# Kernel tuning notes

Hardware: AMD Instinct MI355X
Metric: run time of the kernel (lower is better)

The kernel has to match this reference:

```python
import jax, jax.numpy as jnp
import numpy as np
import math

NX = 240
XL = 6.0
A_ORB = 2
V0 = -20.0
S_INT = 0.5
ITERMAX = 500
FFAC = 0.4


def _wfho(n, x):
    # harmonic-oscillator eigenfunction (numpy, setup only)
    nfac = math.factorial(n)
    norm = (2.0 ** n * nfac) ** (-0.5) / math.pi ** 0.25
    if n == 0:
        Hn = np.ones_like(x)
    elif n == 1:
        Hn = 2.0 * x
    else:
        hm2 = np.ones_like(x)
        hm1 = 2.0 * x
        for m in range(2, n + 1):
            hmx = 2.0 * x * hm1 - 2.0 * (m - 1) * hm2
            hm2, hm1 = hm1, hmx
        Hn = hmx
    return norm * np.exp(-x ** 2 / 2.0) * Hn


def setup_inputs() -> dict:
    delx = 2.0 * XL / NX
    xx = delx * (np.arange(NX) - NX / 2.0)
    delp = 2.0 * math.pi / (2.0 * XL)
    pp = delp * (np.arange(NX) - NX / 2.0)
    # cder2[i,j] = sum_k exp(1j*(xj-xi)*pp_k) * pp_k^2 ; only real part is used
    D = xx[None, :] - xx[:, None]                      # [Nx, Nx], xj - xi
    cder2_re = np.cos(D[:, :, None] * pp[None, None, :]) @ (pp ** 2)
    der2 = -cder2_re * delx * delp / (2.0 * math.pi)
    kin = -der2 / 2.0
    pfac = 1.0 / abs(kin.max())
    U_HO = xx ** 2 / 2.0
    x1, x2 = np.meshgrid(xx, xx, indexing='ij')
    Vint = V0 * (2.0 * math.pi) ** (-0.5) / S_INT * np.exp(-(x1 - x2) ** 2 / (2.0 * S_INT ** 2))
    wfy0 = np.stack([_wfho(n, xx) for n in range(A_ORB)], axis=1)  # [Nx, Nmax]
    return {
        'wfy0': jnp.asarray(wfy0, jnp.float32),
        'kin_mat': jnp.asarray(kin, jnp.float32),
        'Vint': jnp.asarray(Vint, jnp.float32),
        'U_HO': jnp.asarray(U_HO, jnp.float32),
        'delx': jnp.float32(delx),
        'pfac': jnp.float32(pfac),
        'itermax': ITERMAX,
    }


def reference(wfy0, kin_mat, Vint, U_HO, delx, pfac, itermax):
    Nmax = wfy0.shape[1]
    delx = jnp.asarray(delx, jnp.float32).reshape(())
    pfac = jnp.asarray(pfac, jnp.float32).reshape(())

    def step(wfy, _):
        # densities from current orbitals
        hf_den = jnp.sum(wfy ** 2, axis=1)            # [Nx]
        hf_den_mat = wfy @ wfy.T                      # [Nx, Nx]
        Udir = delx * (Vint @ hf_den)
        Umf_mat = -delx * Vint * hf_den_mat
        Umf_mat = Umf_mat + jnp.diag(Udir + U_HO)     # add to diagonal
        H = kin_mat + Umf_mat

        updated = []
        spe = []
        ekin = jnp.float32(0.0)
        epot = jnp.float32(0.0)
        for ieig in range(Nmax):                      # Nmax=2, unrolled
            wf0 = wfy[:, ieig]
            wff = H @ wf0
            spe.append((wf0 @ wff) * delx)
            wfb = wf0 - wff * pfac
            norm = jnp.sum(wfb ** 2) * delx
            wff = wfb / jnp.sqrt(norm)
            for jeig in range(ieig):                  # Gram-Schmidt vs already-updated orbitals
                wff = wff - updated[jeig] * (updated[jeig] @ wff) * delx
            norm = jnp.sum(wff ** 2) * delx
            wff = wff / norm                          # faithful: divide by norm (not sqrt)
            new = FFAC * wff + (1.0 - FFAC) * wf0
            updated.append(new)
            ekin = ekin + (new @ (kin_mat @ new)) * delx
            epot = epot + (new @ (Umf_mat @ new)) * delx
        wfy_new = jnp.stack(updated, axis=1)

        esum0hf = spe[0]
        for s_ in spe[1:]:
            esum0hf = esum0hf + s_
        eho = jnp.sum(hf_den * U_HO) * delx / 2.0
        enerhfp = (esum0hf + ekin) / 2.0 + eho
        epot0hf = epot - 2.0 * eho
        enerhf = esum0hf - epot0hf / 2.0
        out = jnp.stack([enerhf, enerhfp, ekin, eho, epot0hf, esum0hf])
        return wfy_new, out

    _, outs = jax.lax.scan(step, wfy0, None, length=int(itermax))
    return outs[-1]  # (enerhf, enerhfp, ekin0hf, eho, epot0hf, esum0hf)
```

## Files before the change

kernel.cpp:

```cpp
#include <hip/hip_runtime.h>


#define NXX  240
#define NPAD 256
#define NTH  512
#define KJCH 60
#define KNB  15

typedef _Float16 h2 __attribute__((ext_vector_type(2)));

__device__ __forceinline__ h2 bch2(unsigned u) { union { unsigned u; h2 h; } c; c.u = u; return c.h; }
__device__ __forceinline__ unsigned bcu(h2 h)  { union { unsigned u; h2 h; } c; c.h = h; return c.u; }
__device__ __forceinline__ unsigned pkh(float a, float b) {
  h2 p; p.x = (_Float16)a; p.y = (_Float16)b; return bcu(p);
}

__device__ __forceinline__ float fdot2(h2 a, h2 b, float c) {
#if __has_builtin(__builtin_amdgcn_fdot2)
  return __builtin_amdgcn_fdot2(a, b, c, false);
#else
  float d;
  asm("v_dot2_f32_f16 %0, %1, %2, %3" : "=v"(d) : "v"(a), "v"(b), "v"(c));
  return d;
#endif
}

__device__ __forceinline__ float wdw(const float4* w, int idx) {
  const float4 q = w[idx >> 2];
  const int c = idx & 3;
  return c == 0 ? q.x : (c == 1 ? q.y : (c == 2 ? q.z : q.w));
}

template <int CTRL, int N>
__device__ __forceinline__ void dppStepN(float (&v)[N]) {
#pragma unroll
  for (int k = 0; k < N; ++k) {
    int s = __builtin_amdgcn_update_dpp(0, __float_as_int(v[k]), CTRL, 0xF, 0xF, false);
    v[k] += __int_as_float(s);
  }
}
template <int N>
__device__ __forceinline__ void waveSumDppN(float (&v)[N]) {
  dppStepN<0xB1>(v);
  dppStepN<0x4E>(v);
  dppStepN<0x141>(v);
  dppStepN<0x140>(v);
  dppStepN<0x142>(v);
  dppStepN<0x143>(v);
#pragma unroll
  for (int k = 0; k < N; ++k)
    v[k] = __int_as_float(__builtin_amdgcn_readlane(__float_as_int(v[k]), 63));
}

struct __align__(16) Smem {
  float cK[512];
  unsigned pkV[512];
  float uho[NPAD];
  float wfb[2][2][NPAD];
  unsigned xpk[3][NPAD/2];
  unsigned xprk[4][NPAD/2];
  float part[4][6][NPAD];
};

__device__ __forceinline__ void kinConv(const float* x0p, const float* x1p, int jg,
                                        const float4* cw, float (&a0)[4], float (&a1)[4]) {
#pragma unroll
  for (int b = 0; b < KNB; ++b) {
    const int j0 = jg + 4 * b;
    const float4 x0 = *(const float4*)&x0p[j0];
    const float4 x1 = *(const float4*)&x1p[j0];
    const float4 kh = cw[15 - b], kl = cw[14 - b];
    const float ck[8] = {kl.x, kl.y, kl.z, kl.w, kh.x, kh.y, kh.z, kh.w};
    const float xs0[4] = {x0.x, x0.y, x0.z, x0.w};
    const float xs1[4] = {x1.x, x1.y, x1.z, x1.w};
#pragma unroll
    for (int s = 0; s < 4; ++s)
#pragma unroll
      for (int r = 0; r < 4; ++r) {
        const int c = 4 + r - s;
        a0[r] = fmaf(xs0[s], ck[c], a0[r]);
        a1[r] = fmaf(xs1[s], ck[c], a1[r]);
      }
  }
}

template <int NSB>
__device__ __forceinline__ void vConv3(const unsigned* q0, const unsigned* q1,
                                       const unsigned* q2, int jgp,
                                       const float4* win, float (&A)[3][4]) {
#pragma unroll
  for (int sb = 0; sb < NSB; ++sb) {
    const int base = jgp + 4 * sb;
    const uint4 X0 = *(const uint4*)&q0[base];
    const uint4 X1 = *(const uint4*)&q1[base];
    const uint4 X2 = *(const uint4*)&q2[base];
    const unsigned xs0[4] = {X0.x, X0.y, X0.z, X0.w};
    const unsigned xs1[4] = {X1.x, X1.y, X1.z, X1.w};
    const unsigned xs2[4] = {X2.x, X2.y, X2.z, X2.w};
#pragma unroll
    for (int p = 0; p < 4; ++p)
#pragma unroll
      for (int r = 0; r < 4; ++r) {
        const int di = r - 2 * p - 8 * sb + (NSB * 8 - 2) + 2;
        const h2 c = bch2(__float_as_uint(wdw(win, di)));
        A[0][r] = fdot2(c, bch2(xs0[p]), A[0][r]);
        A[1][r] = fdot2(c, bch2(xs1[p]), A[1][r]);
        A[2][r] = fdot2(c, bch2(xs2[p]), A[2][r]);
      }
  }
}

template <int NSB>
__device__ __forceinline__ void vConv4(const unsigned (*q)[NPAD / 2], int jgp,
                                       const float4* win, float (&A)[4][4]) {
#pragma unroll
  for (int sb = 0; sb < NSB; ++sb) {
    const int base = jgp + 4 * sb;
    const uint4 X0 = *(const uint4*)&q[0][base];
    const uint4 X1 = *(const uint4*)&q[1][base];
    const uint4 X2 = *(const uint4*)&q[2][base];
    const uint4 X3 = *(const uint4*)&q[3][base];
    const unsigned xs0[4] = {X0.x, X0.y, X0.z, X0.w};
    const unsigned xs1[4] = {X1.x, X1.y, X1.z, X1.w};
    const unsigned xs2[4] = {X2.x, X2.y, X2.z, X2.w};
    const unsigned xs3[4] = {X3.x, X3.y, X3.z, X3.w};
#pragma unroll
    for (int p = 0; p < 4; ++p)
#pragma unroll
      for (int r = 0; r < 4; ++r) {
        const int di = r - 2 * p - 8 * sb + (NSB * 8 - 2) + 2;
        const h2 c = bch2(__float_as_uint(wdw(win, di)));
        A[0][r] = fdot2(c, bch2(xs0[p]), A[0][r]);
        A[1][r] = fdot2(c, bch2(xs1[p]), A[1][r]);
        A[2][r] = fdot2(c, bch2(xs2[p]), A[2][r]);
        A[3][r] = fdot2(c, bch2(xs3[p]), A[3][r]);
      }
  }
}

__global__ void __launch_bounds__(NTH, 2)
hf_kernel(const float* __restrict__ wfy0,
          const float* __restrict__ kin,
          const float* __restrict__ vnt,
          const float* __restrict__ uho_g,
          const float* __restrict__ delx_p,
          const float* __restrict__ pfac_p,
          const int*   __restrict__ iter_p,
          float* __restrict__ out)
{
  __shared__ Smem sm;
  const int t  = (int)threadIdx.x;
  const int wv = t >> 6;
  const int l  = t & 63;
  const int i0 = 4 * l;
  const bool isK = (wv < 4);
  const int g  = isK ? wv : wv - 4;
  const int jgK = KJCH * g;
  const int jgV = 64 * g;
  const int lenV = (g < 3) ? 64 : 48;
  const float delx = delx_p[0];
  const float pfac = pfac_p[0];
  const int itermax = iter_p[0];

  for (int a = t; a < 512; a += NTH) {
    int d = a - 256;
    float vk = 0.f;
    if (d >= 0 && d < NXX)      vk = kin[(size_t)d * NXX];
    else if (d < 0 && -d < NXX) vk = kin[-d];
    sm.cK[a] = vk;
    float vh = 0.f, vl = 0.f;
    if (d >= 0 && d < NXX)      vh = vnt[(size_t)d * NXX];
    else if (d < 0 && -d < NXX) vh = vnt[-d];
    int d2 = d - 1;
    if (d2 >= 0 && d2 < NXX)      vl = vnt[(size_t)d2 * NXX];
    else if (d2 < 0 && -d2 < NXX) vl = vnt[-d2];
    sm.pkV[a] = pkh(vh, vl);
  }
  if (t < NPAD) {
    float u  = (t < NXX) ? uho_g[t]        : 0.f;
    float a0 = (t < NXX) ? wfy0[2 * t]     : 0.f;
    float a1 = (t < NXX) ? wfy0[2 * t + 1] : 0.f;
    sm.uho[t] = u;
    sm.wfb[0][0][t] = a0; sm.wfb[0][1][t] = a1;
    sm.wfb[1][0][t] = 0.f; sm.wfb[1][1][t] = 0.f;
  }
  if (t < NPAD / 2) {
    int j0 = 2 * t, j1 = 2 * t + 1;
    float w00 = (j0 < NXX) ? wfy0[2 * j0]     : 0.f;
    float w01 = (j0 < NXX) ? wfy0[2 * j0 + 1] : 0.f;
    float w10 = (j1 < NXX) ? wfy0[2 * j1]     : 0.f;
    float w11 = (j1 < NXX) ? wfy0[2 * j1 + 1] : 0.f;
    sm.xpk[0][t] = pkh(w00 * w00, w10 * w10);
    sm.xpk[1][t] = pkh(w00 * w01, w10 * w11);
    sm.xpk[2][t] = pkh(w01 * w01, w11 * w11);
  }
  __syncthreads();

  float4 winq[17];
  if (isK) {
    const int qb = l - 15 * g + 49;
#pragma unroll
    for (int m = 0; m < 16; ++m) winq[m] = *(const float4*)&sm.cK[4 * (qb + m)];
    winq[16] = make_float4(0.f, 0.f, 0.f, 0.f);
  } else {
    const int ab = i0 - jgV - lenV + 256;
#pragma unroll
    for (int m = 0; m < 17; ++m) {
      const uint4 q = *(const uint4*)&sm.pkV[ab + 4 * m];
      winq[m] = make_float4(__uint_as_float(q.x), __uint_as_float(q.y),
                            __uint_as_float(q.z), __uint_as_float(q.w));
    }
  }

  int cur = 0;
  for (int it = 0; it < itermax; ++it) {
    const bool last = (it == itermax - 1);
    const float* wf0 = sm.wfb[cur][0];
    const float* wf1 = sm.wfb[cur][1];
    float* nw0 = sm.wfb[cur ^ 1][0];
    float* nw1 = sm.wfb[cur ^ 1][1];

    if (isK) {
      float aK0[4] = {0, 0, 0, 0}, aK1[4] = {0, 0, 0, 0};
      kinConv(wf0, wf1, jgK, winq, aK0, aK1);
      *(float4*)&sm.part[g][0][i0] = make_float4(aK0[0], aK0[1], aK0[2], aK0[3]);
      *(float4*)&sm.part[g][1][i0] = make_float4(aK1[0], aK1[1], aK1[2], aK1[3]);
    } else {
      float aV[3][4] = {};
      if (g < 3) vConv3<8>(sm.xpk[0], sm.xpk[1], sm.xpk[2], jgV / 2, winq, aV);
      else       vConv3<6>(sm.xpk[0], sm.xpk[1], sm.xpk[2], jgV / 2, winq, aV);
#pragma unroll
      for (int c = 0; c < 3; ++c)
        *(float4*)&sm.part[g][2 + c][i0] =
            make_float4(aV[c][0], aV[c][1], aV[c][2], aV[c][3]);
    }
    __syncthreads();

    float w0[4], w1[4], Ut[4], wff0[4], wff1[4], new0[4], new1[4];
    float spe0 = 0.f, spe1 = 0.f, eho = 0.f;

    if (wv == 0) {
      const bool valid = (l < 60);
      float k0[4]  = {0, 0, 0, 0}, k1[4]  = {0, 0, 0, 0};
      float v00[4] = {0, 0, 0, 0}, v01[4] = {0, 0, 0, 0}, v11[4] = {0, 0, 0, 0};
#pragma unroll
      for (int gg = 0; gg < 4; ++gg) {
        const float4 A0 = *(const float4*)&sm.part[gg][0][i0];
        const float4 A1 = *(const float4*)&sm.part[gg][1][i0];
        const float4 A2 = *(const float4*)&sm.part[gg][2][i0];
        const float4 A3 = *(const float4*)&sm.part[gg][3][i0];
        const float4 A4 = *(const float4*)&sm.part[gg][4][i0];
        k0[0]  += A0.x; k0[1]  += A0.y; k0[2]  += A0.z; k0[3]  += A0.w;
        k1[0]  += A1.x; k1[1]  += A1.y; k1[2]  += A1.z; k1[3]  += A1.w;
        v00[0] += A2.x; v00[1] += A2.y; v00[2] += A2.z; v00[3] += A2.w;
        v01[0] += A3.x; v01[1] += A3.y; v01[2] += A3.z; v01[3] += A3.w;
        v11[0] += A4.x; v11[1] += A4.y; v11[2] += A4.z; v11[3] += A4.w;
      }
      const float4 w0q = *(const float4*)&wf0[i0];
      const float4 w1q = *(const float4*)&wf1[i0];
      const float4 uq  = *(const float4*)&sm.uho[i0];
      w0[0] = w0q.x; w0[1] = w0q.y; w0[2] = w0q.z; w0[3] = w0q.w;
      w1[0] = w1q.x; w1[1] = w1q.y; w1[2] = w1q.z; w1[3] = w1q.w;
      const float uh[4] = {uq.x, uq.y, uq.z, uq.w};

      float wb0[4], wb1[4];
      float red[6] = {0, 0, 0, 0, 0, 0};
#pragma unroll
      for (int r = 0; r < 4; ++r) {
        Ut[r]   = delx * (v00[r] + v11[r]) + uh[r];
        wff0[r] = k0[r] - delx * (w0[r] * v00[r] + w1[r] * v01[r]) + Ut[r] * w0[r];
        wff1[r] = k1[r] - delx * (w0[r] * v01[r] + w1[r] * v11[r]) + Ut[r] * w1[r];
        wb0[r]  = w0[r] - pfac * wff0[r];
        wb1[r]  = w1[r] - pfac * wff1[r];
        if (!valid) { wb0[r] = 0.f; wb1[r] = 0.f; }
        red[0] += wb0[r] * wb0[r];
        red[1] += wb1[r] * wb1[r];
        red[2] += wb0[r] * wb1[r];
        red[3] += w0[r]  * wb1[r];
        red[4] += wb0[r] * w0[r];
        red[5] += w0[r]  * w0[r];
      }
      waveSumDppN<6>(red);
      const float rdelx = 1.f / delx;
      const float inv0 = 1.f / sqrtf(red[0] * delx);
      const float inv1 = 1.f / sqrtf(red[1] * delx);
      const float dB = delx * inv1 * (0.4f * red[2] * inv0 + 0.6f * red[3]);
      const float e0 = 0.16f * rdelx + 0.48f * red[4] * inv0 + 0.36f * red[5];
      const float sB = rdelx - dB * dB * (2.f * rdelx - e0);
      const float invB = 1.f / (sB * delx);
#pragma unroll
      for (int r = 0; r < 4; ++r) {
        const float wfA  = wb0[r] * inv0;
        const float wfBp = wb1[r] * inv1;
        new0[r] = 0.4f * wfA + 0.6f * w0[r];
        const float wfB2 = wfBp - new0[r] * dB;
        new1[r] = 0.4f * wfB2 * invB + 0.6f * w1[r];
      }
      *(float4*)&nw0[i0] = make_float4(new0[0], new0[1], new0[2], new0[3]);
      *(float4*)&nw1[i0] = make_float4(new1[0], new1[1], new1[2], new1[3]);
      *(uint2*)&sm.xpk[0][2 * l] = make_uint2(
          pkh(new0[0] * new0[0], new0[1] * new0[1]),
          pkh(new0[2] * new0[2], new0[3] * new0[3]));
      *(uint2*)&sm.xpk[1][2 * l] = make_uint2(
          pkh(new0[0] * new1[0], new0[1] * new1[1]),
          pkh(new0[2] * new1[2], new0[3] * new1[3]));
      *(uint2*)&sm.xpk[2][2 * l] = make_uint2(
          pkh(new1[0] * new1[0], new1[1] * new1[1]),
          pkh(new1[2] * new1[2], new1[3] * new1[3]));

      if (last) {
        float er[3] = {0, 0, 0};
#pragma unroll
        for (int r = 0; r < 4; ++r) {
          er[0] += w0[r] * wff0[r];
          er[1] += w1[r] * wff1[r];
          er[2] += (w0[r] * w0[r] + w1[r] * w1[r]) * uh[r];
        }
        waveSumDppN<3>(er);
        spe0 = er[0] * delx; spe1 = er[1] * delx; eho = er[2] * delx * 0.5f;
      }
    }
    __syncthreads();

    if (last) {
      if (t < NPAD / 2) {
        const float2 o0 = *(const float2*)&wf0[2 * t];
        const float2 o1 = *(const float2*)&wf1[2 * t];
        const float2 n0 = *(const float2*)&nw0[2 * t];
        const float2 n1 = *(const float2*)&nw1[2 * t];
        sm.xprk[0][t] = pkh(o0.x * n0.x, o0.y * n0.y);
        sm.xprk[1][t] = pkh(o1.x * n0.x, o1.y * n0.y);
        sm.xprk[2][t] = pkh(o0.x * n1.x, o0.y * n1.y);
        sm.xprk[3][t] = pkh(o1.x * n1.x, o1.y * n1.y);
      }
      __syncthreads();

      if (isK) {
        float bA0[4] = {0, 0, 0, 0}, bA1[4] = {0, 0, 0, 0};
        kinConv(nw0, nw1, jgK, winq, bA0, bA1);
        *(float4*)&sm.part[g][0][i0] = make_float4(bA0[0], bA0[1], bA0[2], bA0[3]);
        *(float4*)&sm.part[g][1][i0] = make_float4(bA1[0], bA1[1], bA1[2], bA1[3]);
      } else {
        float bV[4][4] = {};
        if (g < 3) vConv4<8>(sm.xprk, jgV / 2, winq, bV);
        else       vConv4<6>(sm.xprk, jgV / 2, winq, bV);
#pragma unroll
        for (int c2 = 0; c2 < 4; ++c2)
          *(float4*)&sm.part[g][2 + c2][i0] =
              make_float4(bV[c2][0], bV[c2][1], bV[c2][2], bV[c2][3]);
      }
      __syncthreads();

      if (wv == 0) {
        float rd[6][4] = {};
#pragma unroll
        for (int gg = 0; gg < 4; ++gg)
#pragma unroll
          for (int c = 0; c < 6; ++c) {
            const float4 A = *(const float4*)&sm.part[gg][c][i0];
            rd[c][0] += A.x; rd[c][1] += A.y; rd[c][2] += A.z; rd[c][3] += A.w;
          }
        float er[2] = {0, 0};
#pragma unroll
        for (int r = 0; r < 4; ++r) {
          const float um0 = -delx * (w0[r] * rd[2][r] + w1[r] * rd[3][r]) + Ut[r] * new0[r];
          const float um1 = -delx * (w0[r] * rd[4][r] + w1[r] * rd[5][r]) + Ut[r] * new1[r];
          er[0] += new0[r] * rd[0][r] + new1[r] * rd[1][r];
          er[1] += new0[r] * um0 + new1[r] * um1;
        }
        waveSumDppN<2>(er);
        const float ekin = er[0] * delx, epot = er[1] * delx;
        if (l == 0) {
          const float esum    = spe0 + spe1;
          const float enerhfp = 0.5f * (esum + ekin) + eho;
          const float epot0hf = epot - 2.f * eho;
          const float enerhf  = esum - 0.5f * epot0hf;
          out[0] = enerhf; out[1] = enerhfp; out[2] = ekin;
          out[3] = eho;    out[4] = epot0hf; out[5] = esum;
        }
      }
    }
    cur ^= 1;
  }
}

extern "C" void kernel_launch(void* const* d_in, const int* in_sizes, int n_in,
                              void* d_out, int out_size, void* d_ws, size_t ws_size,
                              hipStream_t stream) {
  const float* wfy0 = (const float*)d_in[0];
  const float* kin  = (const float*)d_in[1];
  const float* vnt  = (const float*)d_in[2];
  const float* uho  = (const float*)d_in[3];
  const float* delx = (const float*)d_in[4];
  const float* pfac = (const float*)d_in[5];
  const int*   itm  = (const int*)d_in[6];
  hipLaunchKernelGGL(hf_kernel, dim3(1), dim3(NTH), 0, stream,
                     wfy0, kin, vnt, uho, delx, pfac, itm, (float*)d_out);
}
```

Baseline: 1.079 ms.

## Spread per-iteration orbital update across four waves with cross-wave reductions

Previously a single wave did the whole serial update phase each iteration: summing partials, the Hamiltonian application, Gram-Schmidt and normalization, with four grid points per lane. Now the four kinetic waves each own one point per lane. Their wave-level DPP reductions are combined through a small shared buffer, and the packed fp16 density arrays become per-element halfword stores. This shortens the serial critical path of the update phase and folds the last-iteration product packing into it. The cost is an extra __syncthreads and shared-memory round trips for the cross-wave reductions every iteration.

```diff
diff --git a/kernel.cpp b/kernel.cpp
--- a/kernel.cpp
+++ b/kernel.cpp
@@ -13,6 +13,9 @@
 __device__ __forceinline__ unsigned bcu(h2 h)  { union { unsigned u; h2 h; } c; c.h = h; return c.u; }
 __device__ __forceinline__ unsigned pkh(float a, float b) {
   h2 p; p.x = (_Float16)a; p.y = (_Float16)b; return bcu(p);
+}
+__device__ __forceinline__ unsigned short h16(float a) {
+  union { _Float16 h; unsigned short u; } c; c.h = (_Float16)a; return c.u;
 }
 
 __device__ __forceinline__ float fdot2(h2 a, h2 b, float c) {
@@ -57,9 +60,10 @@
   unsigned pkV[512];
   float uho[NPAD];
   float wfb[2][2][NPAD];
-  unsigned xpk[3][NPAD/2];
-  unsigned xprk[4][NPAD/2];
+  unsigned short xpkh[3][NPAD];
+  unsigned short xprkh[4][NPAD];
   float part[4][6][NPAD];
+  float redb[4][12];
 };
 
 __device__ __forceinline__ void kinConv(const float* x0p, const float* x1p, int jg,
@@ -158,6 +162,7 @@
   const int jgK = KJCH * g;
   const int jgV = 64 * g;
   const int lenV = (g < 3) ? 64 : 48;
+  const int r  = 64 * (wv & 3) + l;
   const float delx = delx_p[0];
   const float pfac = pfac_p[0];
   const int itermax = iter_p[0];
@@ -190,9 +195,9 @@
     float w01 = (j0 < NXX) ? wfy0[2 * j0 + 1] : 0.f;
     float w10 = (j1 < NXX) ? wfy0[2 * j1]     : 0.f;
     float w11 = (j1 < NXX) ? wfy0[2 * j1 + 1] : 0.f;
-    sm.xpk[0][t] = pkh(w00 * w00, w10 * w10);
-    sm.xpk[1][t] = pkh(w00 * w01, w10 * w11);
-    sm.xpk[2][t] = pkh(w01 * w01, w11 * w11);
+    ((unsigned*)sm.xpkh[0])[t] = pkh(w00 * w00, w10 * w10);
+    ((unsigned*)sm.xpkh[1])[t] = pkh(w00 * w01, w10 * w11);
+    ((unsigned*)sm.xpkh[2])[t] = pkh(w01 * w01, w11 * w11);
   }
   __syncthreads();
 
@@ -227,8 +232,10 @@
       *(float4*)&sm.part[g][1][i0] = make_float4(aK1[0], aK1[1], aK1[2], aK1[3]);
     } else {
       float aV[3][4] = {};
-      if (g < 3) vConv3<8>(sm.xpk[0], sm.xpk[1], sm.xpk[2], jgV / 2, winq, aV);
-      else       vConv3<6>(sm.xpk[0], sm.xpk[1], sm.xpk[2], jgV / 2, winq, aV);
+      if (g < 3) vConv3<8>((const unsigned*)sm.xpkh[0], (const unsigned*)sm.xpkh[1],
+                           (const unsigned*)sm.xpkh[2], jgV / 2, winq, aV);
+      else       vConv3<6>((const unsigned*)sm.xpkh[0], (const unsigned*)sm.xpkh[1],
+                           (const unsigned*)sm.xpkh[2], jgV / 2, winq, aV);
 #pragma unroll
       for (int c = 0; c < 3; ++c)
         *(float4*)&sm.part[g][2 + c][i0] =
@@ -236,105 +243,82 @@
     }
     __syncthreads();
 
-    float w0[4], w1[4], Ut[4], wff0[4], wff1[4], new0[4], new1[4];
+    float w0s = 0.f, w1s = 0.f, Uts = 0.f, wff0s = 0.f, wff1s = 0.f;
+    float wb0s = 0.f, wb1s = 0.f, new0s = 0.f, new1s = 0.f;
     float spe0 = 0.f, spe1 = 0.f, eho = 0.f;
 
-    if (wv == 0) {
-      const bool valid = (l < 60);
-      float k0[4]  = {0, 0, 0, 0}, k1[4]  = {0, 0, 0, 0};
-      float v00[4] = {0, 0, 0, 0}, v01[4] = {0, 0, 0, 0}, v11[4] = {0, 0, 0, 0};
+    if (isK) {
+      const bool valid = (r < NXX);
+      float k0 = 0.f, k1 = 0.f, v00 = 0.f, v01 = 0.f, v11 = 0.f;
 #pragma unroll
       for (int gg = 0; gg < 4; ++gg) {
-        const float4 A0 = *(const float4*)&sm.part[gg][0][i0];
-        const float4 A1 = *(const float4*)&sm.part[gg][1][i0];
-        const float4 A2 = *(const float4*)&sm.part[gg][2][i0];
-        const float4 A3 = *(const float4*)&sm.part[gg][3][i0];
-        const float4 A4 = *(const float4*)&sm.part[gg][4][i0];
-        k0[0]  += A0.x; k0[1]  += A0.y; k0[2]  += A0.z; k0[3]  += A0.w;
-        k1[0]  += A1.x; k1[1]  += A1.y; k1[2]  += A1.z; k1[3]  += A1.w;
-        v00[0] += A2.x; v00[1] += A2.y; v00[2] += A2.z; v00[3] += A2.w;
-        v01[0] += A3.x; v01[1] += A3.y; v01[2] += A3.z; v01[3] += A3.w;
-        v11[0] += A4.x; v11[1] += A4.y; v11[2] += A4.z; v11[3] += A4.w;
-      }
-      const float4 w0q = *(const float4*)&wf0[i0];
-      const float4 w1q = *(const float4*)&wf1[i0];
-      const float4 uq  = *(const float4*)&sm.uho[i0];
-      w0[0] = w0q.x; w0[1] = w0q.y; w0[2] = w0q.z; w0[3] = w0q.w;
-      w1[0] = w1q.x; w1[1] = w1q.y; w1[2] = w1q.z; w1[3] = w1q.w;
-      const float uh[4] = {uq.x, uq.y, uq.z, uq.w};
-
-      float wb0[4], wb1[4];
-      float red[6] = {0, 0, 0, 0, 0, 0};
-#pragma unroll
-      for (int r = 0; r < 4; ++r) {
-        Ut[r]   = delx * (v00[r] + v11[r]) + uh[r];
-        wff0[r] = k0[r] - delx * (w0[r] * v00[r] + w1[r] * v01[r]) + Ut[r] * w0[r];
-        wff1[r] = k1[r] - delx * (w0[r] * v01[r] + w1[r] * v11[r]) + Ut[r] * w1[r];
-        wb0[r]  = w0[r] - pfac * wff0[r];
-        wb1[r]  = w1[r] - pfac * wff1[r];
-        if (!valid) { wb0[r] = 0.f; wb1[r] = 0.f; }
-        red[0] += wb0[r] * wb0[r];
-        red[1] += wb1[r] * wb1[r];
-        red[2] += wb0[r] * wb1[r];
-        red[3] += w0[r]  * wb1[r];
-        red[4] += wb0[r] * w0[r];
-        red[5] += w0[r]  * w0[r];
-      }
+        k0  += sm.part[gg][0][r];
+        k1  += sm.part[gg][1][r];
+        v00 += sm.part[gg][2][r];
+        v01 += sm.part[gg][3][r];
+        v11 += sm.part[gg][4][r];
+      }
+      w0s = wf0[r]; w1s = wf1[r];
+      const float uhs = sm.uho[r];
+      Uts   = delx * (v00 + v11) + uhs;
+      wff0s = k0 - delx * (w0s * v00 + w1s * v01) + Uts * w0s;
+      wff1s = k1 - delx * (w0s * v01 + w1s * v11) + Uts * w1s;
+      wb0s  = w0s - pfac * wff0s;
+      wb1s  = w1s - pfac * wff1s;
+      if (!valid) { wb0s = 0.f; wb1s = 0.f; }
+      float red[6] = { wb0s * wb0s, wb1s * wb1s, wb0s * wb1s,
+                       w0s * wb1s,  wb0s * w0s,  w0s * w0s };
       waveSumDppN<6>(red);
+      if (l == 0) {
+#pragma unroll
+        for (int k = 0; k < 6; ++k) sm.redb[wv][k] = red[k];
+      }
+      if (last) {
+        float er[3] = { w0s * wff0s, w1s * wff1s,
+                        (w0s * w0s + w1s * w1s) * uhs };
+        waveSumDppN<3>(er);
+        if (l == 0) {
+          sm.redb[wv][6] = er[0]; sm.redb[wv][7] = er[1]; sm.redb[wv][8] = er[2];
+        }
+      }
+    }
+    __syncthreads();
+
+    if (isK) {
+      float rs[6];
+#pragma unroll
+      for (int k = 0; k < 6; ++k)
+        rs[k] = sm.redb[0][k] + sm.redb[1][k] + sm.redb[2][k] + sm.redb[3][k];
       const float rdelx = 1.f / delx;
-      const float inv0 = 1.f / sqrtf(red[0] * delx);
-      const float inv1 = 1.f / sqrtf(red[1] * delx);
-      const float dB = delx * inv1 * (0.4f * red[2] * inv0 + 0.6f * red[3]);
-      const float e0 = 0.16f * rdelx + 0.48f * red[4] * inv0 + 0.36f * red[5];
+      const float inv0 = 1.f / sqrtf(rs[0] * delx);
+      const float inv1 = 1.f / sqrtf(rs[1] * delx);
+      const float dB = delx * inv1 * (0.4f * rs[2] * inv0 + 0.6f * rs[3]);
+      const float e0 = 0.16f * rdelx + 0.48f * rs[4] * inv0 + 0.36f * rs[5];
       const float sB = rdelx - dB * dB * (2.f * rdelx - e0);
       const float invB = 1.f / (sB * delx);
-#pragma unroll
-      for (int r = 0; r < 4; ++r) {
-        const float wfA  = wb0[r] * inv0;
-        const float wfBp = wb1[r] * inv1;
-        new0[r] = 0.4f * wfA + 0.6f * w0[r];
-        const float wfB2 = wfBp - new0[r] * dB;
-        new1[r] = 0.4f * wfB2 * invB + 0.6f * w1[r];
-      }
-      *(float4*)&nw0[i0] = make_float4(new0[0], new0[1], new0[2], new0[3]);
-      *(float4*)&nw1[i0] = make_float4(new1[0], new1[1], new1[2], new1[3]);
-      *(uint2*)&sm.xpk[0][2 * l] = make_uint2(
-          pkh(new0[0] * new0[0], new0[1] * new0[1]),
-          pkh(new0[2] * new0[2], new0[3] * new0[3]));
-      *(uint2*)&sm.xpk[1][2 * l] = make_uint2(
-          pkh(new0[0] * new1[0], new0[1] * new1[1]),
-          pkh(new0[2] * new1[2], new0[3] * new1[3]));
-      *(uint2*)&sm.xpk[2][2 * l] = make_uint2(
-          pkh(new1[0] * new1[0], new1[1] * new1[1]),
-          pkh(new1[2] * new1[2], new1[3] * new1[3]));
-
+      const float wfA  = wb0s * inv0;
+      const float wfBp = wb1s * inv1;
+      new0s = 0.4f * wfA + 0.6f * w0s;
+      const float wfB2 = wfBp - new0s * dB;
+      new1s = 0.4f * wfB2 * invB + 0.6f * w1s;
+      nw0[r] = new0s;
+      nw1[r] = new1s;
+      sm.xpkh[0][r] = h16(new0s * new0s);
+      sm.xpkh[1][r] = h16(new0s * new1s);
+      sm.xpkh[2][r] = h16(new1s * new1s);
       if (last) {
-        float er[3] = {0, 0, 0};
-#pragma unroll
-        for (int r = 0; r < 4; ++r) {
-          er[0] += w0[r] * wff0[r];
-          er[1] += w1[r] * wff1[r];
-          er[2] += (w0[r] * w0[r] + w1[r] * w1[r]) * uh[r];
-        }
-        waveSumDppN<3>(er);
-        spe0 = er[0] * delx; spe1 = er[1] * delx; eho = er[2] * delx * 0.5f;
+        spe0 = (sm.redb[0][6] + sm.redb[1][6] + sm.redb[2][6] + sm.redb[3][6]) * delx;
+        spe1 = (sm.redb[0][7] + sm.redb[1][7] + sm.redb[2][7] + sm.redb[3][7]) * delx;
+        eho  = (sm.redb[0][8] + sm.redb[1][8] + sm.redb[2][8] + sm.redb[3][8]) * delx * 0.5f;
+        sm.xprkh[0][r] = h16(w0s * new0s);
+        sm.xprkh[1][r] = h16(w1s * new0s);
+        sm.xprkh[2][r] = h16(w0s * new1s);
+        sm.xprkh[3][r] = h16(w1s * new1s);
       }
     }
     __syncthreads();
 
     if (last) {
-      if (t < NPAD / 2) {
-        const float2 o0 = *(const float2*)&wf0[2 * t];
-        const float2 o1 = *(const float2*)&wf1[2 * t];
-        const float2 n0 = *(const float2*)&nw0[2 * t];
-        const float2 n1 = *(const float2*)&nw1[2 * t];
-        sm.xprk[0][t] = pkh(o0.x * n0.x, o0.y * n0.y);
-        sm.xprk[1][t] = pkh(o1.x * n0.x, o1.y * n0.y);
-        sm.xprk[2][t] = pkh(o0.x * n1.x, o0.y * n1.y);
-        sm.xprk[3][t] = pkh(o1.x * n1.x, o1.y * n1.y);
-      }
-      __syncthreads();
-
       if (isK) {
         float bA0[4] = {0, 0, 0, 0}, bA1[4] = {0, 0, 0, 0};
         kinConv(nw0, nw1, jgK, winq, bA0, bA1);
@@ -342,8 +326,10 @@
         *(float4*)&sm.part[g][1][i0] = make_float4(bA1[0], bA1[1], bA1[2], bA1[3]);
       } else {
         float bV[4][4] = {};
-        if (g < 3) vConv4<8>(sm.xprk, jgV / 2, winq, bV);
-        else       vConv4<6>(sm.xprk, jgV / 2, winq, bV);
+        const unsigned (*xq)[NPAD / 2] =
+            reinterpret_cast<const unsigned (*)[NPAD / 2]>(&sm.xprkh[0][0]);
+        if (g < 3) vConv4<8>(xq, jgV / 2, winq, bV);
+        else       vConv4<6>(xq, jgV / 2, winq, bV);
 #pragma unroll
         for (int c2 = 0; c2 < 4; ++c2)
           *(float4*)&sm.part[g][2 + c2][i0] =
@@ -351,33 +337,37 @@
       }
       __syncthreads();
 
-      if (wv == 0) {
-        float rd[6][4] = {};
-#pragma unroll
-        for (int gg = 0; gg < 4; ++gg)
-#pragma unroll
-          for (int c = 0; c < 6; ++c) {
-            const float4 A = *(const float4*)&sm.part[gg][c][i0];
-            rd[c][0] += A.x; rd[c][1] += A.y; rd[c][2] += A.z; rd[c][3] += A.w;
-          }
-        float er[2] = {0, 0};
-#pragma unroll
-        for (int r = 0; r < 4; ++r) {
-          const float um0 = -delx * (w0[r] * rd[2][r] + w1[r] * rd[3][r]) + Ut[r] * new0[r];
-          const float um1 = -delx * (w0[r] * rd[4][r] + w1[r] * rd[5][r]) + Ut[r] * new1[r];
-          er[0] += new0[r] * rd[0][r] + new1[r] * rd[1][r];
-          er[1] += new0[r] * um0 + new1[r] * um1;
+      if (isK) {
+        float kn0 = 0.f, kn1 = 0.f, u00 = 0.f, u01 = 0.f, u10 = 0.f, u11 = 0.f;
+#pragma unroll
+        for (int gg = 0; gg < 4; ++gg) {
+          kn0 += sm.part[gg][0][r];
+          kn1 += sm.part[gg][1][r];
+          u00 += sm.part[gg][2][r];
+          u01 += sm.part[gg][3][r];
+          u10 += sm.part[gg][4][r];
+          u11 += sm.part[gg][5][r];
         }
-        waveSumDppN<2>(er);
-        const float ekin = er[0] * delx, epot = er[1] * delx;
-        if (l == 0) {
-          const float esum    = spe0 + spe1;
-          const float enerhfp = 0.5f * (esum + ekin) + eho;
-          const float epot0hf = epot - 2.f * eho;
-          const float enerhf  = esum - 0.5f * epot0hf;
-          out[0] = enerhf; out[1] = enerhfp; out[2] = ekin;
-          out[3] = eho;    out[4] = epot0hf; out[5] = esum;
-        }
+        const float um0 = -delx * (w0s * u00 + w1s * u01) + Uts * new0s;
+        const float um1 = -delx * (w0s * u10 + w1s * u11) + Uts * new1s;
+        float er2[2] = { new0s * kn0 + new1s * kn1,
+                         new0s * um0 + new1s * um1 };
+        waveSumDppN<2>(er2);
+        if (l == 0) { sm.redb[wv][9] = er2[0]; sm.redb[wv][10] = er2[1]; }
+      }
+      __syncthreads();
+
+      if (t == 0) {
+        const float ekin = (sm.redb[0][9]  + sm.redb[1][9] +
+                            sm.redb[2][9]  + sm.redb[3][9])  * delx;
+        const float epot = (sm.redb[0][10] + sm.redb[1][10] +
+                            sm.redb[2][10] + sm.redb[3][10]) * delx;
+        const float esum    = spe0 + spe1;
+        const float enerhfp = 0.5f * (esum + ekin) + eho;
+        const float epot0hf = epot - 2.f * eho;
+        const float enerhf  = esum - 0.5f * epot0hf;
+        out[0] = enerhf; out[1] = enerhfp; out[2] = ekin;
+        out[3] = eho;    out[4] = epot0hf; out[5] = esum;
       }
     }
     cur ^= 1;
```

Result: slower. 1.120 ms (+3.7%).
